# Kernel tuning notes

Measured on AMD Instinct MI355X. Metric: run time of the kernel, lower is better.

## Reference

```python
import jax, jax.numpy as jnp
import numpy as np

D = 512        # sinusoidal embedding dimension (BoxTerm/PositionTerm input_dimension)
OUT_DIM = 256  # output_dimension
K = 49         # output_size ** 2


def _denoms(c):
    i = np.arange(1, c, 2).astype(np.float64)  # sin exponents
    j = np.arange(0, c, 2).astype(np.float64)  # cos exponents
    return (jnp.asarray(1000.0 ** (i / c), jnp.float32),
            jnp.asarray(1000.0 ** (j / c), jnp.float32))

_DS, _DC = _denoms(D)


def embed(z):
    # z: [...] -> [..., D] ; cat(sin(z/1000^(i/D)) for odd i, cos(z/1000^(j/D)) for even j)
    zz = z[..., None]
    return jnp.concatenate([jnp.sin(zz / _DS), jnp.cos(zz / _DC)], axis=-1)


def setup_inputs() -> dict:
    key = jax.random.key(0)
    ks = jax.random.split(key, 8)
    B, C, H, W, N = 4, 256, 64, 48, 32
    x = jax.random.normal(ks[0], (B, C, H, W), jnp.float32)
    idx = jax.random.randint(ks[1], (N,), 0, B).astype(jnp.float32)
    coords = jax.random.uniform(ks[2], (N, 4), jnp.float32) * 60.0
    rois = jnp.concatenate([idx[:, None], coords], axis=1)  # [N,5]
    s = 0.02  # param scale to keep softmax logits in a sane range
    V_box = jax.random.normal(ks[3], (D, 4 * D), jnp.float32) * s
    W_box = jax.random.normal(ks[4], (K, OUT_DIM, D), jnp.float32) * s
    W_im = jax.random.normal(ks[5], (OUT_DIM, 2 * D), jnp.float32) * s
    conv_w = jax.random.normal(ks[6], (K, C), jnp.float32) * s
    conv_b = jax.random.normal(ks[7], (K,), jnp.float32) * s
    return {"x": x, "rois": rois, "V_box": V_box, "W_box": W_box,
            "W_im": W_im, "conv_w": conv_w, "conv_b": conv_b}


def reference(x, rois, V_box, W_box, W_im, conv_w, conv_b):
    B, C, H, W = x.shape
    N = rois.shape[0]
    idx = rois[:, 0].astype(jnp.int32)              # batch index per box
    coords = rois[:, 1:]                            # [N,4]
    # BoxTerm: eps [N,4D] -> v = V_box @ eps -> per-k W_box_k @ v
    eps = embed(coords).reshape(N, 4 * D)           # [N,4D]
    v = jnp.einsum('df,nf->nd', V_box, eps)         # [N,D]
    bvec = jnp.einsum('kod,nd->nko', W_box, v)      # [N,K,OUT_DIM]
    # PositionTerm: identical for every image -> compute once
    ex = embed(jnp.arange(H, dtype=jnp.float32))    # [H,D]
    ey = embed(jnp.arange(W, dtype=jnp.float32))    # [W,D]
    pos = jnp.concatenate([jnp.broadcast_to(ex[:, None, :], (H, W, D)),
                           jnp.broadcast_to(ey[None, :, :], (H, W, D))], axis=-1)
    img = jnp.einsum('oe,hwe->hwo', W_im, pos)      # [H,W,OUT_DIM]
    # GeometricTerm: per box, per k: (1,OUT_DIM) @ (H,W,OUT_DIM,1)
    geo = jnp.einsum('nko,hwo->nkhw', bvec, img)    # [N,K,H,W]
    # AppearanceTerm: 1x1 conv
    app = jnp.einsum('bchw,oc->bohw', x, conv_w) + conv_b[None, :, None, None]  # [B,K,H,W]
    # LearnableRoIPool: softmax2d(app + geo_box) over channel dim per box
    logits = app[None, :, :, :, :] + geo[:, None, :, :, :]  # [N,B,K,H,W]
    weights = jax.nn.softmax(logits, axis=2)
    # original emits boxes grouped by image index (stable order within image)
    order = jnp.argsort(idx, stable=True)
    return weights[order]
```

## Files before the change

kernel.cpp:

```cpp
#include <hip/hip_runtime.h>

typedef __attribute__((ext_vector_type(8))) short short8;
typedef __attribute__((ext_vector_type(4))) short short4v;
typedef __attribute__((ext_vector_type(4))) float f32x4;

#define LN1000_OVER_512 0.0134917095f

#define IMGB_OFF  0
#define PARTV_OFF 14336
#define BVB_OFF   79872
#define APPT_OFF  280576

__device__ __forceinline__ short f2bf(float x) {
  unsigned u = __float_as_uint(x);
  return (short)((u + 0x7FFFu + ((u >> 16) & 1u)) >> 16);
}
__device__ __forceinline__ short4v f2bf4(float4 v) {
  short4v r; r.x = f2bf(v.x); r.y = f2bf(v.y); r.z = f2bf(v.z); r.w = f2bf(v.w);
  return r;
}

__global__ __launch_bounds__(256) void k1(const float* __restrict__ rois,
                                          const float* __restrict__ W_im,
                                          const float* __restrict__ V_box,
                                          const float* __restrict__ x,
                                          const float* __restrict__ conv_w,
                                          const float* __restrict__ conv_b,
                                          float* __restrict__ ws) {
  __shared__ __align__(16) short sh[96 * 264];
  int bid = blockIdx.x, tid = threadIdx.x;
  int w = tid >> 6, lane = tid & 63;
  int q = lane >> 4, m = lane & 15;

  if (bid < 96) {
    short* Al = sh;
    short* Bl = sh + 32 * 264;
    float inv_s = __expf(-LN1000_OVER_512 * (float)(2 * tid + 1));
    float inv_c = __expf(-LN1000_OVER_512 * (float)(2 * tid));
    f32x4 acc = {0.f, 0.f, 0.f, 0.f};
    int m0 = (w & 1) * 16, n0 = (w >> 1) * 16;

    if (bid < 64) {
      int ntb = bid & 15, ks = bid >> 4;
      int d0 = ntb * 32;
      for (int c = 0; c < 2; ++c) {
        int k0 = ks * 512 + c * 256;
        for (int j = 0; j < 32; ++j) {
          float z = rois[j * 5 + 1 + ks];
          float val = c ? __cosf(z * inv_c) : __sinf(z * inv_s);
          Al[j * 264 + tid] = f2bf(val);
        }
        #pragma unroll
        for (int jj = 0; jj < 8; ++jj) {
          int fid = tid + jj * 256;
          int dd = fid >> 6, k4 = fid & 63;
          float4 v = *(const float4*)(V_box + (size_t)(d0 + dd) * 2048 + k0 + k4 * 4);
          *(short4v*)(Bl + dd * 264 + k4 * 4) = f2bf4(v);
        }
        __syncthreads();
        const short* ap = Al + (m0 + m) * 264 + q * 8;
        const short* bp = Bl + (n0 + m) * 264 + q * 8;
        #pragma unroll
        for (int kk = 0; kk < 8; ++kk) {
          short8 a = *(const short8*)(ap + kk * 32);
          short8 b = *(const short8*)(bp + kk * 32);
          acc = __builtin_amdgcn_mfma_f32_16x16x32_bf16(a, b, acc, 0, 0, 0);
        }
        __syncthreads();
      }
      #pragma unroll
      for (int r = 0; r < 4; ++r)
        ws[PARTV_OFF + ks * 16384 + (m0 + q * 4 + r) * 512 + d0 + n0 + m] = acc[r];
    } else {
      int t = bid - 64;
      int mt = t >> 3, nt = t & 7;
      int rm0 = mt * 32, o0 = nt * 32;
      int khalf = mt >> 1;
      int posbase = rm0 - khalf * 64;
      for (int c = 0; c < 2; ++c) {
        int k0 = khalf * 512 + c * 256;
        for (int j = 0; j < 32; ++j) {
          float z = (float)(posbase + j);
          float val = c ? __cosf(z * inv_c) : __sinf(z * inv_s);
          Al[j * 264 + tid] = f2bf(val);
        }
        #pragma unroll
        for (int jj = 0; jj < 8; ++jj) {
          int fid = tid + jj * 256;
          int dd = fid >> 6, k4 = fid & 63;
          float4 v = *(const float4*)(W_im + (size_t)(o0 + dd) * 1024 + k0 + k4 * 4);
          *(short4v*)(Bl + dd * 264 + k4 * 4) = f2bf4(v);
        }
        __syncthreads();
        const short* ap = Al + (m0 + m) * 264 + q * 8;
        const short* bp = Bl + (n0 + m) * 264 + q * 8;
        #pragma unroll
        for (int kk = 0; kk < 8; ++kk) {
          short8 a = *(const short8*)(ap + kk * 32);
          short8 b = *(const short8*)(bp + kk * 32);
          acc = __builtin_amdgcn_mfma_f32_16x16x32_bf16(a, b, acc, 0, 0, 0);
        }
        __syncthreads();
      }
      short* imgb = (short*)(ws + IMGB_OFF);
      #pragma unroll
      for (int r = 0; r < 4; ++r) {
        int row = rm0 + m0 + q * 4 + r;
        if (row < 112) imgb[row * 256 + o0 + n0 + m] = f2bf(acc[r]);
      }
    }
  } else {
    short* Al = sh;
    short* Bl = sh + 32 * 264;
    int t = bid - 96;
    int b = t / 96, pt = t % 96;
    int p0 = pt * 32;
    const float* xb = x + (size_t)b * 786432;
    #pragma unroll
    for (int j = 0; j < 8; ++j) {
      int fid = tid + j * 256;
      int c = fid >> 3, pj = fid & 7;
      float4 v = *(const float4*)(xb + c * 3072 + p0 + pj * 4);
      Al[(pj * 4 + 0) * 264 + c] = f2bf(v.x);
      Al[(pj * 4 + 1) * 264 + c] = f2bf(v.y);
      Al[(pj * 4 + 2) * 264 + c] = f2bf(v.z);
      Al[(pj * 4 + 3) * 264 + c] = f2bf(v.w);
    }
    #pragma unroll
    for (int j = 0; j < 16; ++j) {
      int fid = tid + j * 256;
      int k = fid >> 6, c4 = fid & 63;
      short4v s4 = {0, 0, 0, 0};
      if (k < 49) s4 = f2bf4(*(const float4*)(conv_w + k * 256 + c4 * 4));
      *(short4v*)(Bl + k * 264 + c4 * 4) = s4;
    }
    __syncthreads();
    int n0 = w * 16;
    f32x4 acc0 = {0.f, 0.f, 0.f, 0.f}, acc1 = {0.f, 0.f, 0.f, 0.f};
    const short* ap = Al + m * 264 + q * 8;
    const short* bp = Bl + (n0 + m) * 264 + q * 8;
    #pragma unroll
    for (int kk = 0; kk < 8; ++kk) {
      short8 b8 = *(const short8*)(bp + kk * 32);
      short8 a0 = *(const short8*)(ap + kk * 32);
      short8 a1 = *(const short8*)(ap + 16 * 264 + kk * 32);
      acc0 = __builtin_amdgcn_mfma_f32_16x16x32_bf16(a0, b8, acc0, 0, 0, 0);
      acc1 = __builtin_amdgcn_mfma_f32_16x16x32_bf16(a1, b8, acc1, 0, 0, 0);
    }
    int k = n0 + m;
    if (k < 49) {
      float bias = conv_b[k];
      float* apt = ws + APPT_OFF + (size_t)b * 159744;
      #pragma unroll
      for (int r = 0; r < 4; ++r) {
        int p = p0 + q * 4 + r;
        apt[(size_t)p * 52 + k] = acc0[r] + bias;
        apt[(size_t)(p + 16) * 52 + k] = acc1[r] + bias;
      }
    }
  }
}

__global__ __launch_bounds__(256) void k2(const float* __restrict__ W_box,
                                          float* __restrict__ ws) {
  __shared__ __align__(16) short Av[32 * 520];
  __shared__ __align__(16) short Bl[32 * 520];
  int tid = threadIdx.x;
  int j0 = blockIdx.x * 32;
  #pragma unroll
  for (int j = 0; j < 16; ++j) {
    int fid = tid + j * 256;
    int n = fid >> 7, d4 = fid & 127;
    const float* p = ws + PARTV_OFF + n * 512 + d4 * 4;
    float4 v0 = *(const float4*)(p);
    float4 v1 = *(const float4*)(p + 16384);
    float4 v2 = *(const float4*)(p + 32768);
    float4 v3 = *(const float4*)(p + 49152);
    float4 s; s.x = v0.x + v1.x + v2.x + v3.x; s.y = v0.y + v1.y + v2.y + v3.y;
    s.z = v0.z + v1.z + v2.z + v3.z; s.w = v0.w + v1.w + v2.w + v3.w;
    *(short4v*)(Av + n * 520 + d4 * 4) = f2bf4(s);
  }
  #pragma unroll
  for (int j = 0; j < 16; ++j) {
    int fid = tid + j * 256;
    int rr = fid >> 7, d4 = fid & 127;
    float4 v = *(const float4*)(W_box + (size_t)(j0 + rr) * 512 + d4 * 4);
    *(short4v*)(Bl + rr * 520 + d4 * 4) = f2bf4(v);
  }
  __syncthreads();
  int w = tid >> 6, lane = tid & 63;
  int q = lane >> 4, m = lane & 15;
  int m0 = (w & 1) * 16, n0 = (w >> 1) * 16;
  f32x4 acc = {0.f, 0.f, 0.f, 0.f};
  const short* ap = Av + (m0 + m) * 520 + q * 8;
  const short* bp = Bl + (n0 + m) * 520 + q * 8;
  #pragma unroll
  for (int kk = 0; kk < 16; ++kk) {
    short8 a = *(const short8*)(ap + kk * 32);
    short8 b = *(const short8*)(bp + kk * 32);
    acc = __builtin_amdgcn_mfma_f32_16x16x32_bf16(a, b, acc, 0, 0, 0);
  }
  short* bvb = (short*)(ws + BVB_OFF);
  #pragma unroll
  for (int r = 0; r < 4; ++r) {
    int row = m0 + q * 4 + r;
    int col = j0 + n0 + m;
    bvb[(size_t)row * 12544 + col] = f2bf(acc[r]);
  }
}

__global__ __launch_bounds__(256) void k3(const float* __restrict__ rois,
                                          const float* __restrict__ ws,
                                          float* __restrict__ out) {
  __shared__ float gxl[64 * 64];
  __shared__ float gyl[64 * 48];
  __shared__ int rank_sh;
  int tid = threadIdx.x, bid = blockIdx.x;
  int n = bid / 12, tile = bid % 12;
  int w = tid >> 6, lane = tid & 63;
  int q = lane >> 4, m = lane & 15;
  const short* bvb  = (const short*)(ws + BVB_OFF);
  const short* imgb = (const short*)(ws + IMGB_OFF);

  if (tid == 0) {
    float my = rois[n * 5];
    int r = 0;
    for (int mm = 0; mm < 32; ++mm) {
      float vm = rois[mm * 5];
      if (vm < my || (vm == my && mm < n)) ++r;
    }
    rank_sh = r;
  }

  for (int t = w; t < 28; t += 4) {
    int kt, rB; bool isy = t >= 16;
    if (!isy) { kt = t >> 2; rB = (t & 3) * 16; }
    else { int tt = t - 16; kt = tt / 3; rB = 64 + (tt % 3) * 16; }
    f32x4 acc = {0.f, 0.f, 0.f, 0.f};
    const short* ap = bvb + ((size_t)n * 49 + kt * 16 + m) * 256 + q * 8;
    const short* bp = imgb + (rB + m) * 256 + q * 8;
    #pragma unroll
    for (int s = 0; s < 8; ++s) {
      short8 a = *(const short8*)(ap + s * 32);
      short8 b = *(const short8*)(bp + s * 32);
      acc = __builtin_amdgcn_mfma_f32_16x16x32_bf16(a, b, acc, 0, 0, 0);
    }
    #pragma unroll
    for (int r = 0; r < 4; ++r) {
      int kk = kt * 16 + q * 4 + r;
      if (!isy) gxl[kk * 64 + rB + m] = acc[r];
      else      gyl[kk * 48 + (rB - 64) + m] = acc[r];
    }
  }
  __syncthreads();

  int pix = tile * 256 + tid;
  int h = pix / 48, wv = pix - h * 48;
  int r = rank_sh;
  for (int b = 0; b < 4; ++b) {
    const float* ap = ws + APPT_OFF + (size_t)(b * 3072 + pix) * 52;
    float lg[49];
    #pragma unroll
    for (int qq = 0; qq < 12; ++qq) {
      float4 tv = *(const float4*)(ap + qq * 4);
      lg[qq * 4 + 0] = tv.x; lg[qq * 4 + 1] = tv.y; lg[qq * 4 + 2] = tv.z; lg[qq * 4 + 3] = tv.w;
    }
    lg[48] = ap[48];
    #pragma unroll
    for (int k = 0; k < 49; ++k)
      lg[k] += gxl[k * 64 + h] + gyl[k * 48 + wv];
    float mx = lg[0];
    #pragma unroll
    for (int k = 1; k < 49; ++k) mx = fmaxf(mx, lg[k]);
    float s = 0.f;
    #pragma unroll
    for (int k = 0; k < 49; ++k) { float e = __expf(lg[k] - mx); lg[k] = e; s += e; }
    float inv = 1.f / s;
    float* op = out + (size_t)(r * 4 + b) * 150528 + pix;
    #pragma unroll
    for (int k = 0; k < 49; ++k)
      op[(size_t)k * 3072] = lg[k] * inv;
  }
}

extern "C" void kernel_launch(void* const* d_in, const int* in_sizes, int n_in,
                              void* d_out, int out_size, void* d_ws, size_t ws_size,
                              hipStream_t stream) {
  const float* x      = (const float*)d_in[0];
  const float* rois   = (const float*)d_in[1];
  const float* V_box  = (const float*)d_in[2];
  const float* W_box  = (const float*)d_in[3];
  const float* W_im   = (const float*)d_in[4];
  const float* conv_w = (const float*)d_in[5];
  const float* conv_b = (const float*)d_in[6];
  float* ws  = (float*)d_ws;
  float* out = (float*)d_out;

  hipLaunchKernelGGL(k1, dim3(480), dim3(256), 0, stream, rois, W_im, V_box, x, conv_w, conv_b, ws);
  hipLaunchKernelGGL(k2, dim3(392), dim3(256), 0, stream, W_box, ws);
  hipLaunchKernelGGL(k3, dim3(384), dim3(256), 0, stream, rois, ws, out);
}
```

Before: 156.7 us.

## Split geometric GEMM into separate kernel and parallelize softmax over batch

The per-box geometric projection (bvec times image embedding) moves out of the softmax kernel into its own MFMA kernel. That kernel writes gx/gy tables to the workspace, so they are no longer recomputed redundantly by each of the 12 tiles per box. The softmax kernel now launches one block per (box, batch, tile), giving 1536 blocks instead of 384, and loads only the gx slice its tile needs. This trades an extra launch and a workspace round trip for more parallelism and less redundant MFMA work.

```diff
diff --git a/kernel.cpp b/kernel.cpp
--- a/kernel.cpp
+++ b/kernel.cpp
@@ -10,6 +10,8 @@
 #define PARTV_OFF 14336
 #define BVB_OFF   79872
 #define APPT_OFF  280576
+#define GX_OFF    919552
+#define GY_OFF    1019904
 
 __device__ __forceinline__ short f2bf(float x) {
   unsigned u = __float_as_uint(x);
@@ -209,19 +211,73 @@
   }
 }
 
-__global__ __launch_bounds__(256) void k3(const float* __restrict__ rois,
+__global__ __launch_bounds__(256) void k3(float* __restrict__ ws) {
+  __shared__ __align__(16) short Al[32 * 264];
+  int tid = threadIdx.x;
+  int half = blockIdx.x & 1, rb = blockIdx.x >> 1;
+  int r0 = rb * 32;
+  const short* bvb = (const short*)(ws + BVB_OFF);
+  #pragma unroll
+  for (int j = 0; j < 4; ++j) {
+    int fid = tid + j * 256;
+    int rr = fid >> 5, o8 = fid & 31;
+    *(short8*)(Al + rr * 264 + o8 * 8) = *(const short8*)(bvb + (size_t)(r0 + rr) * 256 + o8 * 8);
+  }
+  __syncthreads();
+  int w = tid >> 6, lane = tid & 63;
+  int q = lane >> 4, m = lane & 15;
+  int nct = half ? 3 : 4;
+  if (w < nct) {
+    const short* imgb = (const short*)(ws + IMGB_OFF) + (half ? 64 * 256 : 0);
+    int ct = w;
+    f32x4 acc0 = {0.f, 0.f, 0.f, 0.f}, acc1 = {0.f, 0.f, 0.f, 0.f};
+    const short* ap0 = Al + m * 264 + q * 8;
+    const short* ap1 = Al + (16 + m) * 264 + q * 8;
+    const short* bp  = imgb + (ct * 16 + m) * 256 + q * 8;
+    #pragma unroll
+    for (int kk = 0; kk < 8; ++kk) {
+      short8 b8 = *(const short8*)(bp + kk * 32);
+      short8 a0 = *(const short8*)(ap0 + kk * 32);
+      short8 a1 = *(const short8*)(ap1 + kk * 32);
+      acc0 = __builtin_amdgcn_mfma_f32_16x16x32_bf16(a0, b8, acc0, 0, 0, 0);
+      acc1 = __builtin_amdgcn_mfma_f32_16x16x32_bf16(a1, b8, acc1, 0, 0, 0);
+    }
+    float* outp = ws + (half ? GY_OFF : GX_OFF);
+    int stride = half ? 48 : 64;
+    int col = ct * 16 + m;
+    #pragma unroll
+    for (int r = 0; r < 4; ++r) {
+      outp[(r0 + q * 4 + r) * stride + col]      = acc0[r];
+      outp[(r0 + 16 + q * 4 + r) * stride + col] = acc1[r];
+    }
+  }
+}
+
+__global__ __launch_bounds__(256) void k4(const float* __restrict__ rois,
                                           const float* __restrict__ ws,
                                           float* __restrict__ out) {
-  __shared__ float gxl[64 * 64];
-  __shared__ float gyl[64 * 48];
+  __shared__ float gyl[2352];
+  __shared__ float gxs[392];
   __shared__ int rank_sh;
   int tid = threadIdx.x, bid = blockIdx.x;
-  int n = bid / 12, tile = bid % 12;
-  int w = tid >> 6, lane = tid & 63;
-  int q = lane >> 4, m = lane & 15;
-  const short* bvb  = (const short*)(ws + BVB_OFF);
-  const short* imgb = (const short*)(ws + IMGB_OFF);
-
+  int n = bid / 48;
+  int rem = bid % 48;
+  int b = rem / 12, tile = rem % 12;
+  int h0 = (tile * 256) / 48;
+  #pragma unroll
+  for (int j = 0; j < 3; ++j) {
+    int id = tid + j * 256;
+    if (id < 588) *(float4*)(gyl + id * 4) = *(const float4*)(ws + GY_OFF + n * 2352 + id * 4);
+  }
+  #pragma unroll
+  for (int j = 0; j < 2; ++j) {
+    int id = tid + j * 256;
+    if (id < 392) {
+      int row = id >> 3, c = id & 7;
+      int col = h0 + c; if (col > 63) col = 63;
+      gxs[id] = ws[GX_OFF + (n * 49 + row) * 64 + col];
+    }
+  }
   if (tid == 0) {
     float my = rois[n * 5];
     int r = 0;
@@ -231,56 +287,32 @@
     }
     rank_sh = r;
   }
-
-  for (int t = w; t < 28; t += 4) {
-    int kt, rB; bool isy = t >= 16;
-    if (!isy) { kt = t >> 2; rB = (t & 3) * 16; }
-    else { int tt = t - 16; kt = tt / 3; rB = 64 + (tt % 3) * 16; }
-    f32x4 acc = {0.f, 0.f, 0.f, 0.f};
-    const short* ap = bvb + ((size_t)n * 49 + kt * 16 + m) * 256 + q * 8;
-    const short* bp = imgb + (rB + m) * 256 + q * 8;
-    #pragma unroll
-    for (int s = 0; s < 8; ++s) {
-      short8 a = *(const short8*)(ap + s * 32);
-      short8 b = *(const short8*)(bp + s * 32);
-      acc = __builtin_amdgcn_mfma_f32_16x16x32_bf16(a, b, acc, 0, 0, 0);
-    }
-    #pragma unroll
-    for (int r = 0; r < 4; ++r) {
-      int kk = kt * 16 + q * 4 + r;
-      if (!isy) gxl[kk * 64 + rB + m] = acc[r];
-      else      gyl[kk * 48 + (rB - 64) + m] = acc[r];
-    }
-  }
   __syncthreads();
-
   int pix = tile * 256 + tid;
   int h = pix / 48, wv = pix - h * 48;
-  int r = rank_sh;
-  for (int b = 0; b < 4; ++b) {
-    const float* ap = ws + APPT_OFF + (size_t)(b * 3072 + pix) * 52;
-    float lg[49];
-    #pragma unroll
-    for (int qq = 0; qq < 12; ++qq) {
-      float4 tv = *(const float4*)(ap + qq * 4);
-      lg[qq * 4 + 0] = tv.x; lg[qq * 4 + 1] = tv.y; lg[qq * 4 + 2] = tv.z; lg[qq * 4 + 3] = tv.w;
-    }
-    lg[48] = ap[48];
-    #pragma unroll
-    for (int k = 0; k < 49; ++k)
-      lg[k] += gxl[k * 64 + h] + gyl[k * 48 + wv];
-    float mx = lg[0];
-    #pragma unroll
-    for (int k = 1; k < 49; ++k) mx = fmaxf(mx, lg[k]);
-    float s = 0.f;
-    #pragma unroll
-    for (int k = 0; k < 49; ++k) { float e = __expf(lg[k] - mx); lg[k] = e; s += e; }
-    float inv = 1.f / s;
-    float* op = out + (size_t)(r * 4 + b) * 150528 + pix;
-    #pragma unroll
-    for (int k = 0; k < 49; ++k)
-      op[(size_t)k * 3072] = lg[k] * inv;
-  }
+  int dh = h - h0;
+  float lg[49];
+  const float* ap = ws + APPT_OFF + (size_t)(b * 3072 + pix) * 52;
+  #pragma unroll
+  for (int qq = 0; qq < 12; ++qq) {
+    float4 tv = *(const float4*)(ap + qq * 4);
+    lg[qq * 4 + 0] = tv.x; lg[qq * 4 + 1] = tv.y; lg[qq * 4 + 2] = tv.z; lg[qq * 4 + 3] = tv.w;
+  }
+  lg[48] = ap[48];
+  #pragma unroll
+  for (int k = 0; k < 49; ++k)
+    lg[k] += gxs[k * 8 + dh] + gyl[k * 48 + wv];
+  float mx = lg[0];
+  #pragma unroll
+  for (int k = 1; k < 49; ++k) mx = fmaxf(mx, lg[k]);
+  float s = 0.f;
+  #pragma unroll
+  for (int k = 0; k < 49; ++k) { float e = __expf(lg[k] - mx); lg[k] = e; s += e; }
+  float inv = 1.f / s;
+  float* op = out + (size_t)(rank_sh * 4 + b) * 150528 + pix;
+  #pragma unroll
+  for (int k = 0; k < 49; ++k)
+    op[(size_t)k * 3072] = lg[k] * inv;
 }
 
 extern "C" void kernel_launch(void* const* d_in, const int* in_sizes, int n_in,
@@ -296,7 +328,8 @@
   float* ws  = (float*)d_ws;
   float* out = (float*)d_out;
 
-  hipLaunchKernelGGL(k1, dim3(480), dim3(256), 0, stream, rois, W_im, V_box, x, conv_w, conv_b, ws);
-  hipLaunchKernelGGL(k2, dim3(392), dim3(256), 0, stream, W_box, ws);
-  hipLaunchKernelGGL(k3, dim3(384), dim3(256), 0, stream, rois, ws, out);
-}
+  hipLaunchKernelGGL(k1, dim3(480),  dim3(256), 0, stream, rois, W_im, V_box, x, conv_w, conv_b, ws);
+  hipLaunchKernelGGL(k2, dim3(392),  dim3(256), 0, stream, W_box, ws);
+  hipLaunchKernelGGL(k3, dim3(98),   dim3(256), 0, stream, ws);
+  hipLaunchKernelGGL(k4, dim3(1536), dim3(256), 0, stream, rois, ws, out);
+}
```

Result: faster. 143.8 us (-8.3%).
